# Kernel optimization log

Measured on AMD Instinct MI355X. Metric: run time of the kernel, lower is better.

## Reference

```python
import jax, jax.numpy as jnp
import numpy as np

D_MODEL, HEAD_DIM = 1024, 128

def setup_inputs() -> dict:
    key = jax.random.key(0)
    kx, kq, kk, kv = jax.random.split(key, 4)
    x = jax.random.normal(kx, (4, 4096, D_MODEL), dtype=jnp.float32)
    s = 1.0 / np.sqrt(D_MODEL)
    Wq = jax.random.normal(kq, (D_MODEL, HEAD_DIM), dtype=jnp.float32) * s
    Wk = jax.random.normal(kk, (D_MODEL, HEAD_DIM), dtype=jnp.float32) * s
    Wv = jax.random.normal(kv, (D_MODEL, HEAD_DIM), dtype=jnp.float32) * s
    return {"x": x, "Wq": Wq, "Wk": Wk, "Wv": Wv}

def reference(x, Wq, Wk, Wv):
    # x: [b, s, d_model]; Wq/Wk/Wv: [d_model, head_dim]
    q = jnp.einsum('bsd,dh->bsh', x, Wq)
    k = jnp.einsum('bsd,dh->bsh', x, Wk)
    v = jnp.einsum('bsd,dh->bsh', x, Wv)
    seq = x.shape[1]
    scale = 1.0 / jnp.sqrt(jnp.asarray(q.shape[-1], q.dtype))
    scores = jnp.einsum('bqh,bkh->bqk', q, k) * scale  # [b, s, s]
    causal = jnp.tril(jnp.ones((seq, seq), dtype=bool))
    scores = jnp.where(causal, scores, jnp.asarray(-jnp.inf, scores.dtype))
    attn = jax.nn.softmax(scores, axis=-1)
    return jnp.einsum('bqk,bkh->bqh', attn, v)
```

## Files before the change

### kernel.cpp

```cpp
#include <hip/hip_runtime.h>
#include <hip/hip_bf16.h>
#include <math.h>

#define D_MODEL 1024
#define HD 128
#define SEQ 4096

typedef __bf16 bf16x8 __attribute__((ext_vector_type(8)));
typedef float f32x4 __attribute__((ext_vector_type(4)));
typedef unsigned int u32;
typedef u32 u32x4 __attribute__((ext_vector_type(4)));

__device__ __forceinline__ unsigned short f2bf(float f) {
    union { float f; u32 u; } c; c.f = f;
    u32 u = c.u;
    u = (u + 0x7fffu + ((u >> 16) & 1u)) >> 16;
    return (unsigned short)u;
}
__device__ __forceinline__ u32 pk2(float a, float b) {
    __hip_bfloat162 h = __float22bfloat162_rn(make_float2(a, b));
    union { __hip_bfloat162 h; u32 u; } c; c.h = h; return c.u;
}
__device__ __forceinline__ void dma16(void* lds, const void* g) {
    __builtin_amdgcn_global_load_lds(
        (const __attribute__((address_space(1))) u32*)g,
        (__attribute__((address_space(3))) u32*)lds, 16, 0, 0);
}
__device__ __forceinline__ void drain_dma()  { __builtin_amdgcn_s_waitcnt(0x0F70); }
__device__ __forceinline__ void drain_dma4() { __builtin_amdgcn_s_waitcnt(0x0F74); }

__global__ __launch_bounds__(256)
void wt_kernel(const float* __restrict__ Wq, const float* __restrict__ Wk,
               const float* __restrict__ Wv, unsigned short* __restrict__ Wt) {
    __shared__ float wsf[64][129];
    const int t = threadIdx.x;
    const int k0 = blockIdx.x * 64;
    const int mat = blockIdx.y;
    const float* W = (mat == 0) ? Wq : (mat == 1) ? Wk : Wv;
    const float sc = (mat == 0) ? (0.08838834764831845f * 1.4426950408889634f) : 1.0f;
    {
        const int r = t >> 2, c = (t & 3) * 32;
        const float* src = W + (size_t)(k0 + r) * HD + c;
        #pragma unroll
        for (int j = 0; j < 32; j += 4)
            *reinterpret_cast<f32x4*>(&wsf[r][c + j]) = *reinterpret_cast<const f32x4*>(src + j);
    }
    __syncthreads();
    const int n = t >> 1, ks = (t & 1) * 32;
    u32 ow[16];
    #pragma unroll
    for (int j = 0; j < 16; ++j)
        ow[j] = pk2(wsf[ks + 2 * j][n] * sc, wsf[ks + 2 * j + 1][n] * sc);
    unsigned short* dst = Wt + (size_t)(mat * HD + n) * D_MODEL + k0 + ks;
    #pragma unroll
    for (int j = 0; j < 4; ++j)
        *reinterpret_cast<u32x4*>(dst + j * 8) = (u32x4){ow[4*j], ow[4*j+1], ow[4*j+2], ow[4*j+3]};
}

__global__ __launch_bounds__(256)
void proj_kernel(const float* __restrict__ x, const unsigned short* __restrict__ Wt,
                 unsigned short* __restrict__ Qb, unsigned short* __restrict__ Kb,
                 unsigned short* __restrict__ Vt) {
    __shared__ __align__(1024) char ps[49152];
    const int t = threadIdx.x;
    const int w = t >> 6, l = t & 63, li = l & 15, g2 = l >> 4;
    const int id = blockIdx.x;
    const int grp = id / 24, win = id % 24;
    const int nbase = (win >> 3) * 128;
    const int rowbase = (grp * 8 + (win & 7)) * 64;

    f32x4 acc[8];
    #pragma unroll
    for (int nt = 0; nt < 8; ++nt) acc[nt] = (f32x4){0.f, 0.f, 0.f, 0.f};

    const int lrow = l >> 3;
    const int xg = (l & 7) ^ (lrow & 6);
    const int wgr = (l & 7) ^ lrow;
    const int wrow_add = (wgr >> 2) << 6;
    const int wkc = (wgr & 3) * 8;

    auto stage = [&](int k0, int buf) {
        #pragma unroll
        for (int j = 0; j < 2; ++j) {
            int r0 = w * 16 + 8 * j;
            dma16(ps + buf * 8192 + r0 * 128,
                  x + (size_t)(rowbase + r0 + lrow) * D_MODEL + k0 + xg * 4);
            dma16(ps + 24576 + buf * 8192 + r0 * 128,
                  Wt + (size_t)(nbase + r0 + lrow + wrow_add) * D_MODEL + k0 + wkc);
        }
    };

    stage(0, 0);
    stage(32, 1);
    for (int it = 0; it < 32; ++it) {
        const int buf = it % 3;
        if (it < 31) drain_dma4(); else drain_dma();
        __syncthreads();
        if (it + 2 < 32) stage((it + 2) * 32, (it + 2) % 3);
        const char* xb = ps + buf * 8192 + (w * 16 + li) * 128 + (((2 * g2) ^ (li & 6)) * 16);
        f32x4 x0 = *reinterpret_cast<const f32x4*>(xb);
        f32x4 x1 = *reinterpret_cast<const f32x4*>(xb + 16);
        union { u32 d[4]; bf16x8 v; } cva;
        cva.d[0] = pk2(x0[0], x0[1]); cva.d[1] = pk2(x0[2], x0[3]);
        cva.d[2] = pk2(x1[0], x1[1]); cva.d[3] = pk2(x1[2], x1[3]);
        bf16x8 af = cva.v;
        #pragma unroll
        for (int nt = 0; nt < 8; ++nt) {
            bf16x8 bfr = *reinterpret_cast<const bf16x8*>(
                ps + 24576 + buf * 8192 + ((nt & 3) * 16 + li) * 128 +
                ((((nt >> 2) * 4 + g2) ^ (li & 7)) * 16));
            acc[nt] = __builtin_amdgcn_mfma_f32_16x16x32_bf16(af, bfr, acc[nt], 0, 0, 0);
        }
    }

    if (nbase < 256) {
        unsigned short* P = nbase ? Kb : Qb;
        #pragma unroll
        for (int nt = 0; nt < 8; ++nt)
            #pragma unroll
            for (int r = 0; r < 4; ++r) {
                int grow = rowbase + w * 16 + g2 * 4 + r;
                P[(size_t)grow * HD + nt * 16 + li] = f2bf(acc[nt][r]);
            }
    } else {
        int grow0 = rowbase + w * 16 + g2 * 4;
        int b_ = grow0 >> 12, s_ = grow0 & 4095;
        #pragma unroll
        for (int nt = 0; nt < 8; ++nt) {
            ushort4 s4;
            s4.x = f2bf(acc[nt][0]); s4.y = f2bf(acc[nt][1]);
            s4.z = f2bf(acc[nt][2]); s4.w = f2bf(acc[nt][3]);
            *reinterpret_cast<ushort4*>(&Vt[((size_t)b_ * HD + nt * 16 + li) * SEQ + s_]) = s4;
        }
    }
}

__global__ __launch_bounds__(256, 2)
void attn_kernel(const unsigned short* __restrict__ Qb, const unsigned short* __restrict__ Kb,
                 const unsigned short* __restrict__ Vt, float* __restrict__ outO,
                 unsigned short* __restrict__ Obf, float* __restrict__ Lbuf) {
    __shared__ __align__(1024) char smem[73728];
    const int t = threadIdx.x;
    const int w = t >> 6, l = t & 63, li = l & 15, g2 = l >> 4;
    const int qh = w >> 1, kh = w & 1;
    const int b = blockIdx.x & 3;
    const int u = blockIdx.x >> 2;
    const int g = 63 - (u >> 2);
    const int c = u & 3;
    const int R = g + 1;
    const int ts = (c * R) >> 2, te = ((c + 1) * R) >> 2;
    const int q0 = g * 64;
    const size_t rowb = (size_t)b * SEQ;
    const int koff = kh * 32;

    const unsigned short* KbB = Kb + rowb * HD;
    const unsigned short* VtB = Vt + (size_t)b * HD * SEQ;
    const int vgran = ((l & 7) ^ (l >> 3)) * 8;

    auto stage = [&](int it, char* base) {
        const int j0 = it * 64;
        #pragma unroll
        for (int j = 0; j < 4; ++j) {
            int rK = w * 16 + 4 * j + (l >> 4);
            dma16(base + (w * 16 + 4 * j) * 256,
                  KbB + (size_t)(j0 + rK) * 128 + (((l & 15) ^ (rK & 7)) * 8));
            int rV = w * 32 + 8 * j + (l >> 3);
            dma16(base + 16384 + (w * 32 + 8 * j) * 128,
                  VtB + (size_t)rV * SEQ + j0 + vgran);
        }
    };

    bf16x8 qf[2][4];
    #pragma unroll
    for (int qt = 0; qt < 2; ++qt)
        #pragma unroll
        for (int ks = 0; ks < 4; ++ks)
            qf[qt][ks] = *reinterpret_cast<const bf16x8*>(
                Qb + (rowb + q0 + qh * 32 + qt * 16 + li) * HD + ks * 32 + g2 * 8);

    f32x4 acco[2][8];
    #pragma unroll
    for (int qt = 0; qt < 2; ++qt)
        #pragma unroll
        for (int dt = 0; dt < 8; ++dt) acco[qt][dt] = (f32x4){0.f, 0.f, 0.f, 0.f};
    float ls[2] = {0.f, 0.f};

    const int gV = ((4 * kh + g2) ^ (li & 7)) * 16;

    if (ts < te) stage(ts, smem);
    for (int it = ts; it < te; ++it) {
        char* cbuf = smem + ((it - ts) & 1) * 32768;
        char* nbuf = smem + (((it - ts) & 1) ^ 1) * 32768;
        drain_dma();
        __syncthreads();
        if (it + 1 < te) stage(it + 1, nbuf);

        f32x4 accs[2][2];
        #pragma unroll
        for (int qt = 0; qt < 2; ++qt)
            #pragma unroll
            for (int kt = 0; kt < 2; ++kt) accs[qt][kt] = (f32x4){0.f, 0.f, 0.f, 0.f};
        #pragma unroll
        for (int kt = 0; kt < 2; ++kt) {
            const char* kb = cbuf + (koff + kt * 16 + li) * 256;
            #pragma unroll
            for (int ks = 0; ks < 4; ++ks) {
                bf16x8 kf = *reinterpret_cast<const bf16x8*>(kb + (((4 * ks + g2) ^ (li & 7)) * 16));
                accs[0][kt] = __builtin_amdgcn_mfma_f32_16x16x32_bf16(kf, qf[0][ks], accs[0][kt], 0, 0, 0);
                accs[1][kt] = __builtin_amdgcn_mfma_f32_16x16x32_bf16(kf, qf[1][ks], accs[1][kt], 0, 0, 0);
            }
        }

        const bool masked = (it == g);
        #pragma unroll
        for (int qt = 0; qt < 2; ++qt) {
            const int prow = qh * 32 + qt * 16 + li;
            #pragma unroll
            for (int kt = 0; kt < 2; ++kt) {
                float p[4];
                #pragma unroll
                for (int r = 0; r < 4; ++r) {
                    float s = accs[qt][kt][r];
                    if (masked && (koff + kt * 16 + g2 * 4 + r > prow)) s = -INFINITY;
                    p[r] = __builtin_amdgcn_exp2f(s - 16.0f);
                    ls[qt] += p[r];
                }
                union { u32 d[2]; uint2 v; } pw;
                pw.d[0] = pk2(p[0], p[1]); pw.d[1] = pk2(p[2], p[3]);
                int gr = (kh * 4 + kt * 2 + (g2 >> 1)) ^ (prow & 7);
                *reinterpret_cast<uint2*>(
                    smem + 65536 + prow * 128 + gr * 16 + (g2 & 1) * 8) = pw.v;
            }
        }

        bf16x8 pb[2];
        #pragma unroll
        for (int qt = 0; qt < 2; ++qt) {
            const int prow = qh * 32 + qt * 16 + li;
            pb[qt] = *reinterpret_cast<const bf16x8*>(
                smem + 65536 + prow * 128 + (((kh * 4 + g2) ^ (prow & 7)) * 16));
        }
        #pragma unroll
        for (int dt = 0; dt < 8; ++dt) {
            bf16x8 va = *reinterpret_cast<const bf16x8*>(cbuf + 16384 + (dt * 16 + li) * 128 + gV);
            acco[0][dt] = __builtin_amdgcn_mfma_f32_16x16x32_bf16(va, pb[0], acco[0][dt], 0, 0, 0);
            acco[1][dt] = __builtin_amdgcn_mfma_f32_16x16x32_bf16(va, pb[1], acco[1][dt], 0, 0, 0);
        }
    }

    #pragma unroll
    for (int qt = 0; qt < 2; ++qt) {
        ls[qt] += __shfl_xor(ls[qt], 16);
        ls[qt] += __shfl_xor(ls[qt], 32);
    }

    float (*Osum)[132] = (float(*)[132])smem;
    float* Lsh = (float*)(smem + 33792);
    __syncthreads();
    if (l < 16) {
        Lsh[kh * 64 + qh * 32 + l]      = ls[0];
        Lsh[kh * 64 + qh * 32 + 16 + l] = ls[1];
    }
    if (kh == 0) {
        #pragma unroll
        for (int qt = 0; qt < 2; ++qt)
            #pragma unroll
            for (int dt = 0; dt < 8; ++dt)
                *reinterpret_cast<f32x4*>(
                    &Osum[qh * 32 + qt * 16 + li][dt * 16 + g2 * 4]) = acco[qt][dt];
    }
    __syncthreads();
    if (kh == 1) {
        #pragma unroll
        for (int qt = 0; qt < 2; ++qt)
            #pragma unroll
            for (int dt = 0; dt < 8; ++dt) {
                f32x4* p = reinterpret_cast<f32x4*>(
                    &Osum[qh * 32 + qt * 16 + li][dt * 16 + g2 * 4]);
                f32x4 v = *p;
                #pragma unroll
                for (int j = 0; j < 4; ++j) v[j] += acco[qt][dt][j];
                *p = v;
            }
    }
    __syncthreads();

    if (t < 64)
        Lbuf[(size_t)c * 16384 + rowb + q0 + t] = Lsh[t] + Lsh[64 + t];
    #pragma unroll
    for (int k = 0; k < 8; ++k) {
        int idx = t + k * 256;
        int row = idx >> 5, col = (idx & 31) * 4;
        f32x4 o = *reinterpret_cast<const f32x4*>(&Osum[row][col]);
        size_t grow = rowb + q0 + row;
        if (c == 3) {
            *reinterpret_cast<f32x4*>(&outO[grow * HD + col]) = o;
        } else {
            union { u32 d[2]; uint2 v; } pkd;
            pkd.d[0] = pk2(o[0], o[1]); pkd.d[1] = pk2(o[2], o[3]);
            *reinterpret_cast<uint2*>(&Obf[(size_t)c * 2097152 + grow * HD + col]) = pkd.v;
        }
    }
}

__global__ __launch_bounds__(256)
void merge_kernel(float* __restrict__ outO, const unsigned short* __restrict__ Obf,
                  const float* __restrict__ Lbuf) {
    int tid = blockIdx.x * 256 + threadIdx.x;
    #pragma unroll
    for (int k = 0; k < 4; ++k) {
        int idx = tid + k * 131072;
        int row = idx >> 5, col = (idx & 31) * 4;
        float lsum = Lbuf[row] + Lbuf[16384 + row] + Lbuf[32768 + row] + Lbuf[49152 + row];
        float inv = 1.f / lsum;
        f32x4 o = *reinterpret_cast<const f32x4*>(&outO[(size_t)row * HD + col]);
        #pragma unroll
        for (int cc = 0; cc < 3; ++cc) {
            ushort4 uu = *reinterpret_cast<const ushort4*>(
                &Obf[(size_t)cc * 2097152 + (size_t)row * HD + col]);
            union { u32 u; float f; } a, b2, c2, d2;
            a.u = (u32)uu.x << 16; b2.u = (u32)uu.y << 16;
            c2.u = (u32)uu.z << 16; d2.u = (u32)uu.w << 16;
            o[0] += a.f; o[1] += b2.f; o[2] += c2.f; o[3] += d2.f;
        }
        #pragma unroll
        for (int j = 0; j < 4; ++j) o[j] *= inv;
        *reinterpret_cast<f32x4*>(&outO[(size_t)row * HD + col]) = o;
    }
}

extern "C" void kernel_launch(void* const* d_in, const int* in_sizes, int n_in,
                              void* d_out, int out_size, void* d_ws, size_t ws_size,
                              hipStream_t stream) {
    const float* x  = (const float*)d_in[0];
    const float* Wq = (const float*)d_in[1];
    const float* Wk = (const float*)d_in[2];
    const float* Wv = (const float*)d_in[3];
    float* out = (float*)d_out;

    char* ws = (char*)d_ws;
    unsigned short* Qb  = (unsigned short*)(ws);
    unsigned short* Kb  = (unsigned short*)(ws + ((size_t)4  << 20));
    unsigned short* Vt  = (unsigned short*)(ws + ((size_t)8  << 20));
    unsigned short* Wt  = (unsigned short*)(ws + ((size_t)12 << 20));
    unsigned short* Obf = (unsigned short*)(ws + ((size_t)13 << 20));
    float*          Lb  = (float*)(ws + ((size_t)25 << 20));

    wt_kernel   <<<dim3(16, 3), dim3(256), 0, stream>>>(Wq, Wk, Wv, Wt);
    proj_kernel <<<dim3(768),   dim3(256), 0, stream>>>(x, Wt, Qb, Kb, Vt);
    attn_kernel <<<dim3(1024),  dim3(256), 0, stream>>>(Qb, Kb, Vt, out, Obf, Lb);
    merge_kernel<<<dim3(512),   dim3(256), 0, stream>>>(out, Obf, Lb);
}
```

Baseline: 165.9 us.

## Pre-swizzle weights into MFMA fragment layout and drop LDS staging in projection

The weight prep kernel now writes the bf16 weights already arranged in per-lane MFMA B-fragment order, so each lane can fetch its fragment with one contiguous 16-byte global load. The projection kernel removes its triple-buffered LDS pipeline (async global-to-LDS copies, waitcnts, barriers) and reads x and weight fragments straight from global memory. The aim is to cut the synchronisation and LDS traffic. The cost is losing explicit prefetch and latency hiding, and relying on the cache for the weight reuse that LDS sharing used to provide across waves.

```diff
diff --git a/kernel.cpp b/kernel.cpp
--- a/kernel.cpp
+++ b/kernel.cpp
@@ -27,11 +27,10 @@
         (__attribute__((address_space(3))) u32*)lds, 16, 0, 0);
 }
 __device__ __forceinline__ void drain_dma()  { __builtin_amdgcn_s_waitcnt(0x0F70); }
-__device__ __forceinline__ void drain_dma4() { __builtin_amdgcn_s_waitcnt(0x0F74); }
 
 __global__ __launch_bounds__(256)
 void wt_kernel(const float* __restrict__ Wq, const float* __restrict__ Wk,
-               const float* __restrict__ Wv, unsigned short* __restrict__ Wt) {
+               const float* __restrict__ Wv, unsigned short* __restrict__ Wt2) {
     __shared__ float wsf[64][129];
     const int t = threadIdx.x;
     const int k0 = blockIdx.x * 64;
@@ -46,69 +45,58 @@
             *reinterpret_cast<f32x4*>(&wsf[r][c + j]) = *reinterpret_cast<const f32x4*>(src + j);
     }
     __syncthreads();
-    const int n = t >> 1, ks = (t & 1) * 32;
-    u32 ow[16];
-    #pragma unroll
-    for (int j = 0; j < 16; ++j)
-        ow[j] = pk2(wsf[ks + 2 * j][n] * sc, wsf[ks + 2 * j + 1][n] * sc);
-    unsigned short* dst = Wt + (size_t)(mat * HD + n) * D_MODEL + k0 + ks;
-    #pragma unroll
-    for (int j = 0; j < 4; ++j)
-        *reinterpret_cast<u32x4*>(dst + j * 8) = (u32x4){ow[4*j], ow[4*j+1], ow[4*j+2], ow[4*j+3]};
+    const int l = t & 63, sub = t >> 6;
+    const int li = l & 15, g2 = l >> 4;
+    #pragma unroll
+    for (int nt2 = 0; nt2 < 2; ++nt2) {
+        const int nt = sub * 2 + nt2;
+        const int n = nt * 16 + li;
+        #pragma unroll
+        for (int ksl = 0; ksl < 2; ++ksl) {
+            const int ks = (k0 >> 5) + ksl;
+            u32 ow[4];
+            #pragma unroll
+            for (int jj = 0; jj < 4; ++jj) {
+                int kl = ksl * 32 + g2 * 8 + 2 * jj;
+                ow[jj] = pk2(wsf[kl][n] * sc, wsf[kl + 1][n] * sc);
+            }
+            *reinterpret_cast<u32x4*>(
+                Wt2 + (size_t)((mat * 8 + nt) * 32 + ks) * 512 + l * 8) =
+                (u32x4){ow[0], ow[1], ow[2], ow[3]};
+        }
+    }
 }
 
 __global__ __launch_bounds__(256)
-void proj_kernel(const float* __restrict__ x, const unsigned short* __restrict__ Wt,
+void proj_kernel(const float* __restrict__ x, const unsigned short* __restrict__ Wt2,
                  unsigned short* __restrict__ Qb, unsigned short* __restrict__ Kb,
                  unsigned short* __restrict__ Vt) {
-    __shared__ __align__(1024) char ps[49152];
     const int t = threadIdx.x;
     const int w = t >> 6, l = t & 63, li = l & 15, g2 = l >> 4;
     const int id = blockIdx.x;
     const int grp = id / 24, win = id % 24;
-    const int nbase = (win >> 3) * 128;
+    const int slice = win >> 3;
+    const int nbase = slice * 128;
     const int rowbase = (grp * 8 + (win & 7)) * 64;
 
     f32x4 acc[8];
     #pragma unroll
     for (int nt = 0; nt < 8; ++nt) acc[nt] = (f32x4){0.f, 0.f, 0.f, 0.f};
 
-    const int lrow = l >> 3;
-    const int xg = (l & 7) ^ (lrow & 6);
-    const int wgr = (l & 7) ^ lrow;
-    const int wrow_add = (wgr >> 2) << 6;
-    const int wkc = (wgr & 3) * 8;
-
-    auto stage = [&](int k0, int buf) {
-        #pragma unroll
-        for (int j = 0; j < 2; ++j) {
-            int r0 = w * 16 + 8 * j;
-            dma16(ps + buf * 8192 + r0 * 128,
-                  x + (size_t)(rowbase + r0 + lrow) * D_MODEL + k0 + xg * 4);
-            dma16(ps + 24576 + buf * 8192 + r0 * 128,
-                  Wt + (size_t)(nbase + r0 + lrow + wrow_add) * D_MODEL + k0 + wkc);
-        }
-    };
-
-    stage(0, 0);
-    stage(32, 1);
+    const float* xrow = x + (size_t)(rowbase + w * 16 + li) * D_MODEL + g2 * 8;
+    const unsigned short* wbase = Wt2 + (size_t)(slice * 8) * 32 * 512 + l * 8;
+
+    #pragma unroll 2
     for (int it = 0; it < 32; ++it) {
-        const int buf = it % 3;
-        if (it < 31) drain_dma4(); else drain_dma();
-        __syncthreads();
-        if (it + 2 < 32) stage((it + 2) * 32, (it + 2) % 3);
-        const char* xb = ps + buf * 8192 + (w * 16 + li) * 128 + (((2 * g2) ^ (li & 6)) * 16);
-        f32x4 x0 = *reinterpret_cast<const f32x4*>(xb);
-        f32x4 x1 = *reinterpret_cast<const f32x4*>(xb + 16);
+        f32x4 x0 = *reinterpret_cast<const f32x4*>(xrow + it * 32);
+        f32x4 x1 = *reinterpret_cast<const f32x4*>(xrow + it * 32 + 4);
         union { u32 d[4]; bf16x8 v; } cva;
         cva.d[0] = pk2(x0[0], x0[1]); cva.d[1] = pk2(x0[2], x0[3]);
         cva.d[2] = pk2(x1[0], x1[1]); cva.d[3] = pk2(x1[2], x1[3]);
         bf16x8 af = cva.v;
         #pragma unroll
         for (int nt = 0; nt < 8; ++nt) {
-            bf16x8 bfr = *reinterpret_cast<const bf16x8*>(
-                ps + 24576 + buf * 8192 + ((nt & 3) * 16 + li) * 128 +
-                ((((nt >> 2) * 4 + g2) ^ (li & 7)) * 16));
+            bf16x8 bfr = *reinterpret_cast<const bf16x8*>(wbase + (size_t)(nt * 32 + it) * 512);
             acc[nt] = __builtin_amdgcn_mfma_f32_16x16x32_bf16(af, bfr, acc[nt], 0, 0, 0);
         }
     }
@@ -342,12 +330,12 @@
     unsigned short* Qb  = (unsigned short*)(ws);
     unsigned short* Kb  = (unsigned short*)(ws + ((size_t)4  << 20));
     unsigned short* Vt  = (unsigned short*)(ws + ((size_t)8  << 20));
-    unsigned short* Wt  = (unsigned short*)(ws + ((size_t)12 << 20));
+    unsigned short* Wt2 = (unsigned short*)(ws + ((size_t)12 << 20));
     unsigned short* Obf = (unsigned short*)(ws + ((size_t)13 << 20));
     float*          Lb  = (float*)(ws + ((size_t)25 << 20));
 
-    wt_kernel   <<<dim3(16, 3), dim3(256), 0, stream>>>(Wq, Wk, Wv, Wt);
-    proj_kernel <<<dim3(768),   dim3(256), 0, stream>>>(x, Wt, Qb, Kb, Vt);
+    wt_kernel   <<<dim3(16, 3), dim3(256), 0, stream>>>(Wq, Wk, Wv, Wt2);
+    proj_kernel <<<dim3(768),   dim3(256), 0, stream>>>(x, Wt2, Qb, Kb, Vt);
     attn_kernel <<<dim3(1024),  dim3(256), 0, stream>>>(Qb, Kb, Vt, out, Obf, Lb);
     merge_kernel<<<dim3(512),   dim3(256), 0, stream>>>(out, Obf, Lb);
 }
```

Result: slower. 181.3 us (+9.3%).

## Give each wave its own query rows and shrink key tiles to 32

Applied to the files above, without the earlier changes.

The attention kernel previously split work across waves as 2 query-halves x 2 key-halves, which forced a cross-wave reduction of O and L through shared memory at the end. Now each of the 4 waves owns 16 query rows and processes all keys, using 32-key tiles (twice as many iterations) with halved LDS buffers. Each wave writes its output directly, and the epilogue syncs and shared-memory reduction are gone. In exchange, each K/V tile is reused by only 16 query rows per wave, there are twice as many barriers per block, and the MFMA work per barrier shrinks.

```diff
diff --git a/kernel.cpp b/kernel.cpp
--- a/kernel.cpp
+++ b/kernel.cpp
@@ -139,166 +139,109 @@
 void attn_kernel(const unsigned short* __restrict__ Qb, const unsigned short* __restrict__ Kb,
                  const unsigned short* __restrict__ Vt, float* __restrict__ outO,
                  unsigned short* __restrict__ Obf, float* __restrict__ Lbuf) {
-    __shared__ __align__(1024) char smem[73728];
+    __shared__ __align__(1024) char smem[36864];
     const int t = threadIdx.x;
     const int w = t >> 6, l = t & 63, li = l & 15, g2 = l >> 4;
-    const int qh = w >> 1, kh = w & 1;
     const int b = blockIdx.x & 3;
     const int u = blockIdx.x >> 2;
     const int g = 63 - (u >> 2);
     const int c = u & 3;
-    const int R = g + 1;
+    const int R = 2 * g + 2;
     const int ts = (c * R) >> 2, te = ((c + 1) * R) >> 2;
     const int q0 = g * 64;
     const size_t rowb = (size_t)b * SEQ;
-    const int koff = kh * 32;
+    const int qloc = w * 16 + li;
 
     const unsigned short* KbB = Kb + rowb * HD;
     const unsigned short* VtB = Vt + (size_t)b * HD * SEQ;
-    const int vgran = ((l & 7) ^ (l >> 3)) * 8;
 
     auto stage = [&](int it, char* base) {
-        const int j0 = it * 64;
-        #pragma unroll
-        for (int j = 0; j < 4; ++j) {
-            int rK = w * 16 + 4 * j + (l >> 4);
-            dma16(base + (w * 16 + 4 * j) * 256,
-                  KbB + (size_t)(j0 + rK) * 128 + (((l & 15) ^ (rK & 7)) * 8));
-            int rV = w * 32 + 8 * j + (l >> 3);
-            dma16(base + 16384 + (w * 32 + 8 * j) * 128,
-                  VtB + (size_t)rV * SEQ + j0 + vgran);
+        const int j0 = it * 32;
+        #pragma unroll
+        for (int j = 0; j < 2; ++j) {
+            int rK = w * 8 + 4 * j + (l >> 4);
+            dma16(base + (w * 8 + 4 * j) * 256,
+                  KbB + (size_t)(j0 + rK) * HD + (((l & 15) ^ (rK & 7)) * 8));
+            int rV = w * 32 + 16 * j + (l >> 2);
+            dma16(base + 8192 + (w * 32 + 16 * j) * 64,
+                  VtB + (size_t)rV * SEQ + j0 + (((l & 3) ^ ((l >> 4) & 3)) * 8));
         }
     };
 
-    bf16x8 qf[2][4];
-    #pragma unroll
-    for (int qt = 0; qt < 2; ++qt)
-        #pragma unroll
-        for (int ks = 0; ks < 4; ++ks)
-            qf[qt][ks] = *reinterpret_cast<const bf16x8*>(
-                Qb + (rowb + q0 + qh * 32 + qt * 16 + li) * HD + ks * 32 + g2 * 8);
-
-    f32x4 acco[2][8];
-    #pragma unroll
-    for (int qt = 0; qt < 2; ++qt)
-        #pragma unroll
-        for (int dt = 0; dt < 8; ++dt) acco[qt][dt] = (f32x4){0.f, 0.f, 0.f, 0.f};
-    float ls[2] = {0.f, 0.f};
-
-    const int gV = ((4 * kh + g2) ^ (li & 7)) * 16;
+    bf16x8 qf[4];
+    #pragma unroll
+    for (int ks = 0; ks < 4; ++ks)
+        qf[ks] = *reinterpret_cast<const bf16x8*>(
+            Qb + (rowb + q0 + qloc) * HD + ks * 32 + g2 * 8);
+
+    f32x4 acco[8];
+    #pragma unroll
+    for (int dt = 0; dt < 8; ++dt) acco[dt] = (f32x4){0.f, 0.f, 0.f, 0.f};
+    float ls = 0.f;
 
     if (ts < te) stage(ts, smem);
     for (int it = ts; it < te; ++it) {
-        char* cbuf = smem + ((it - ts) & 1) * 32768;
-        char* nbuf = smem + (((it - ts) & 1) ^ 1) * 32768;
+        char* cbuf = smem + ((it - ts) & 1) * 16384;
+        char* nbuf = smem + (((it - ts) & 1) ^ 1) * 16384;
         drain_dma();
         __syncthreads();
         if (it + 1 < te) stage(it + 1, nbuf);
 
-        f32x4 accs[2][2];
-        #pragma unroll
-        for (int qt = 0; qt < 2; ++qt)
-            #pragma unroll
-            for (int kt = 0; kt < 2; ++kt) accs[qt][kt] = (f32x4){0.f, 0.f, 0.f, 0.f};
+        f32x4 accs[2] = {{0.f,0.f,0.f,0.f}, {0.f,0.f,0.f,0.f}};
         #pragma unroll
         for (int kt = 0; kt < 2; ++kt) {
-            const char* kb = cbuf + (koff + kt * 16 + li) * 256;
+            const char* kb = cbuf + (kt * 16 + li) * 256;
             #pragma unroll
             for (int ks = 0; ks < 4; ++ks) {
                 bf16x8 kf = *reinterpret_cast<const bf16x8*>(kb + (((4 * ks + g2) ^ (li & 7)) * 16));
-                accs[0][kt] = __builtin_amdgcn_mfma_f32_16x16x32_bf16(kf, qf[0][ks], accs[0][kt], 0, 0, 0);
-                accs[1][kt] = __builtin_amdgcn_mfma_f32_16x16x32_bf16(kf, qf[1][ks], accs[1][kt], 0, 0, 0);
+                accs[kt] = __builtin_amdgcn_mfma_f32_16x16x32_bf16(kf, qf[ks], accs[kt], 0, 0, 0);
             }
         }
 
-        const bool masked = (it == g);
-        #pragma unroll
-        for (int qt = 0; qt < 2; ++qt) {
-            const int prow = qh * 32 + qt * 16 + li;
+        const bool masked = (it >= 2 * g);
+        #pragma unroll
+        for (int kt = 0; kt < 2; ++kt) {
+            float p[4];
             #pragma unroll
-            for (int kt = 0; kt < 2; ++kt) {
-                float p[4];
-                #pragma unroll
-                for (int r = 0; r < 4; ++r) {
-                    float s = accs[qt][kt][r];
-                    if (masked && (koff + kt * 16 + g2 * 4 + r > prow)) s = -INFINITY;
-                    p[r] = __builtin_amdgcn_exp2f(s - 16.0f);
-                    ls[qt] += p[r];
-                }
-                union { u32 d[2]; uint2 v; } pw;
-                pw.d[0] = pk2(p[0], p[1]); pw.d[1] = pk2(p[2], p[3]);
-                int gr = (kh * 4 + kt * 2 + (g2 >> 1)) ^ (prow & 7);
-                *reinterpret_cast<uint2*>(
-                    smem + 65536 + prow * 128 + gr * 16 + (g2 & 1) * 8) = pw.v;
+            for (int r = 0; r < 4; ++r) {
+                float s = accs[kt][r];
+                if (masked && ((it - 2 * g) * 32 + kt * 16 + g2 * 4 + r > qloc)) s = -INFINITY;
+                p[r] = __builtin_amdgcn_exp2f(s - 16.0f);
+                ls += p[r];
             }
-        }
-
-        bf16x8 pb[2];
-        #pragma unroll
-        for (int qt = 0; qt < 2; ++qt) {
-            const int prow = qh * 32 + qt * 16 + li;
-            pb[qt] = *reinterpret_cast<const bf16x8*>(
-                smem + 65536 + prow * 128 + (((kh * 4 + g2) ^ (prow & 7)) * 16));
-        }
+            union { u32 d[2]; uint2 v; } pw;
+            pw.d[0] = pk2(p[0], p[1]); pw.d[1] = pk2(p[2], p[3]);
+            int gq = kt * 2 + (g2 >> 1);
+            *reinterpret_cast<uint2*>(
+                smem + 32768 + qloc * 64 + ((gq ^ (li & 3)) * 16) + (g2 & 1) * 8) = pw.v;
+        }
+
+        bf16x8 pb = *reinterpret_cast<const bf16x8*>(
+            smem + 32768 + qloc * 64 + ((g2 ^ (li & 3)) * 16));
         #pragma unroll
         for (int dt = 0; dt < 8; ++dt) {
-            bf16x8 va = *reinterpret_cast<const bf16x8*>(cbuf + 16384 + (dt * 16 + li) * 128 + gV);
-            acco[0][dt] = __builtin_amdgcn_mfma_f32_16x16x32_bf16(va, pb[0], acco[0][dt], 0, 0, 0);
-            acco[1][dt] = __builtin_amdgcn_mfma_f32_16x16x32_bf16(va, pb[1], acco[1][dt], 0, 0, 0);
-        }
-    }
-
-    #pragma unroll
-    for (int qt = 0; qt < 2; ++qt) {
-        ls[qt] += __shfl_xor(ls[qt], 16);
-        ls[qt] += __shfl_xor(ls[qt], 32);
-    }
-
-    float (*Osum)[132] = (float(*)[132])smem;
-    float* Lsh = (float*)(smem + 33792);
-    __syncthreads();
-    if (l < 16) {
-        Lsh[kh * 64 + qh * 32 + l]      = ls[0];
-        Lsh[kh * 64 + qh * 32 + 16 + l] = ls[1];
-    }
-    if (kh == 0) {
-        #pragma unroll
-        for (int qt = 0; qt < 2; ++qt)
-            #pragma unroll
-            for (int dt = 0; dt < 8; ++dt)
-                *reinterpret_cast<f32x4*>(
-                    &Osum[qh * 32 + qt * 16 + li][dt * 16 + g2 * 4]) = acco[qt][dt];
-    }
-    __syncthreads();
-    if (kh == 1) {
-        #pragma unroll
-        for (int qt = 0; qt < 2; ++qt)
-            #pragma unroll
-            for (int dt = 0; dt < 8; ++dt) {
-                f32x4* p = reinterpret_cast<f32x4*>(
-                    &Osum[qh * 32 + qt * 16 + li][dt * 16 + g2 * 4]);
-                f32x4 v = *p;
-                #pragma unroll
-                for (int j = 0; j < 4; ++j) v[j] += acco[qt][dt][j];
-                *p = v;
-            }
-    }
-    __syncthreads();
-
-    if (t < 64)
-        Lbuf[(size_t)c * 16384 + rowb + q0 + t] = Lsh[t] + Lsh[64 + t];
-    #pragma unroll
-    for (int k = 0; k < 8; ++k) {
-        int idx = t + k * 256;
-        int row = idx >> 5, col = (idx & 31) * 4;
-        f32x4 o = *reinterpret_cast<const f32x4*>(&Osum[row][col]);
-        size_t grow = rowb + q0 + row;
+            bf16x8 va = *reinterpret_cast<const bf16x8*>(
+                cbuf + 8192 + (dt * 16 + li) * 64 + ((g2 ^ (li >> 2)) * 16));
+            acco[dt] = __builtin_amdgcn_mfma_f32_16x16x32_bf16(va, pb, acco[dt], 0, 0, 0);
+        }
+    }
+
+    ls += __shfl_xor(ls, 16);
+    ls += __shfl_xor(ls, 32);
+    if (l < 16)
+        Lbuf[(size_t)c * 16384 + rowb + q0 + w * 16 + l] = ls;
+
+    const size_t qrow = rowb + q0 + qloc;
+    #pragma unroll
+    for (int dt = 0; dt < 8; ++dt) {
         if (c == 3) {
-            *reinterpret_cast<f32x4*>(&outO[grow * HD + col]) = o;
+            *reinterpret_cast<f32x4*>(&outO[qrow * HD + dt * 16 + g2 * 4]) = acco[dt];
         } else {
             union { u32 d[2]; uint2 v; } pkd;
-            pkd.d[0] = pk2(o[0], o[1]); pkd.d[1] = pk2(o[2], o[3]);
-            *reinterpret_cast<uint2*>(&Obf[(size_t)c * 2097152 + grow * HD + col]) = pkd.v;
+            pkd.d[0] = pk2(acco[dt][0], acco[dt][1]);
+            pkd.d[1] = pk2(acco[dt][2], acco[dt][3]);
+            *reinterpret_cast<uint2*>(
+                &Obf[(size_t)c * 2097152 + qrow * HD + dt * 16 + g2 * 4]) = pkd.v;
         }
     }
 }
```

Result: slower. 171.8 us (+3.5%).
